# Kernel tuning notes

Hardware: AMD Instinct MI355X
Metric: run time of the kernel (lower is better)

Reference implementation:

```python
import jax, jax.numpy as jnp
import numpy as np

IN_F, OUT_F, GROUP, BITS = 4096, 11008, 128, 4
PACK = 32 // BITS            # 8 nibbles per int32 word
N_GROUPS = IN_F // GROUP     # 32
MASK = (1 << BITS) - 1       # 0xF
TOKENS = 2048


def setup_inputs() -> dict:
    key = jax.random.key(0)
    ks = jax.random.split(key, 6)
    x = jax.random.normal(ks[0], (TOKENS, IN_F), dtype=jnp.float32)
    qweight = jax.random.randint(ks[1], (IN_F // PACK, OUT_F), 0, 2147483647, dtype=jnp.int32)
    qzeros = jax.random.randint(ks[2], (N_GROUPS, OUT_F // PACK), 0, 2147483647, dtype=jnp.int32)
    qscales = jax.random.randint(ks[3], (N_GROUPS, OUT_F), 0, 256, dtype=jnp.int32)  # uint8 values
    qscales_zeros = jax.random.uniform(ks[4], (1, OUT_F), dtype=jnp.float32)
    qscales_scales = jax.random.uniform(ks[5], (1, OUT_F), dtype=jnp.float32) * 0.01
    g_idx = jnp.arange(IN_F, dtype=jnp.int32) // GROUP
    return dict(x=x, qweight=qweight, qzeros=qzeros, qscales=qscales,
                qscales_zeros=qscales_zeros, qscales_scales=qscales_scales, g_idx=g_idx)


def _dequantize(qweight, qzeros, qscales, qscales_zeros, qscales_scales, g_idx, dtype):
    shifts = jnp.arange(0, 32, BITS, dtype=jnp.int32)  # [8]
    # unpack weights: [in/8, 8, out] -> [in, out]
    w = (qweight[:, None, :] >> shifts[None, :, None]) & MASK
    w = w.reshape(-1, qweight.shape[-1])
    # unpack zero-points (+1 per original code): [n_groups, out/8, 8] -> [n_groups, out]
    z = (((qzeros[:, :, None] >> shifts[None, None, :]) & MASK) + 1)
    z = z.reshape(-1, qweight.shape[-1])
    # dequantize the uint8-quantized scales, then apply group-wise
    scales = (qscales.astype(dtype) - qscales_zeros) * qscales_scales  # [n_groups, out]
    return (w - z[g_idx]).astype(dtype) * scales[g_idx]                # [in, out]


def reference(x, qweight, qzeros, qscales, qscales_zeros, qscales_scales, g_idx):
    weight = _dequantize(qweight, qzeros, qscales, qscales_zeros, qscales_scales,
                         g_idx, x.dtype)
    return x @ weight  # bias disabled (disable_bias=True)
```

## Files before the change

### kernel.cpp

```cpp
#include <hip/hip_runtime.h>
#include <hip/hip_fp16.h>
#include <stdint.h>

#define IN_F   4096
#define OUT_F  11008
#define TOKENS 2048
#define BM 128
#define BN 64
#define BK 64
#define NT (IN_F / BK)
#define NGROUP 32
#define OPW (OUT_F / 8)

typedef _Float16 f16;
typedef __attribute__((ext_vector_type(2))) _Float16 f16x2;
typedef __attribute__((ext_vector_type(8))) _Float16 f16x8;
typedef __attribute__((ext_vector_type(4))) float f32x4;
typedef __attribute__((ext_vector_type(4))) int   i32x4;

typedef __attribute__((address_space(3))) uint32_t lds_u32_t;
typedef const __attribute__((address_space(1))) uint32_t glb_u32_t;

#define SB0() __builtin_amdgcn_sched_barrier(0)

static __device__ __forceinline__ void gload_lds16(const void* g, void* l) {
    __builtin_amdgcn_global_load_lds((glb_u32_t*)g, (lds_u32_t*)l, 16, 0, 0);
}

__global__ __launch_bounds__(256) void quant_x_kernel(const float* __restrict__ x,
                                                      char* __restrict__ xi,
                                                      float* __restrict__ aws) {
    __shared__ float red[4];
    const int row = blockIdx.x;
    const int tid = threadIdx.x;
    const float* xr = x + (size_t)row * IN_F + tid * 16;
    float v[16];
    #pragma unroll
    for (int p = 0; p < 4; ++p) {
        const float4 t = *reinterpret_cast<const float4*>(xr + p * 4);
        v[p * 4 + 0] = t.x; v[p * 4 + 1] = t.y; v[p * 4 + 2] = t.z; v[p * 4 + 3] = t.w;
    }
    float m = 0.f;
    #pragma unroll
    for (int p = 0; p < 16; ++p) m = fmaxf(m, fabsf(v[p]));
    #pragma unroll
    for (int off = 32; off > 0; off >>= 1) m = fmaxf(m, __shfl_xor(m, off));
    if ((tid & 63) == 0) red[tid >> 6] = m;
    __syncthreads();
    m = fmaxf(fmaxf(red[0], red[1]), fmaxf(red[2], red[3]));
    const float a   = m * (1.0f / 127.0f);
    const float inv = (m > 0.f) ? 127.0f / m : 0.f;
    if (tid == 0) aws[row] = a;
    const float MAGIC = 12582912.0f;
    uint32_t b[16];
    #pragma unroll
    for (int p = 0; p < 16; ++p)
        b[p] = __builtin_bit_cast(uint32_t, fmaf(v[p], inv, MAGIC)) & 0xFFu;
    i32x4 d;
    d[0] = (int)(b[0] | (b[2] << 8) | (b[4]  << 16) | (b[6]  << 24));
    d[1] = (int)(b[1] | (b[3] << 8) | (b[5]  << 16) | (b[7]  << 24));
    d[2] = (int)(b[8] | (b[10] << 8) | (b[12] << 16) | (b[14] << 24));
    d[3] = (int)(b[9] | (b[11] << 8) | (b[13] << 16) | (b[15] << 24));
    *reinterpret_cast<i32x4*>(xi + (size_t)row * IN_F + tid * 16) = d;
}

__global__ __launch_bounds__(256, 4) void qgemm_i8_kernel(
    const char*     __restrict__ xi,
    const float*    __restrict__ aws,
    const uint32_t* __restrict__ qweight,
    const uint32_t* __restrict__ qzeros,
    const int*      __restrict__ qscales,
    const float*    __restrict__ qscales_zeros,
    const float*    __restrict__ qscales_scales,
    float*          __restrict__ out)
{
    __shared__ __align__(16) char Ash[2][BM * BK];
    __shared__ __align__(16) char Bsh[2][BN * BK];

    const int tid  = threadIdx.x;
    const int lane = tid & 63;
    const int wid  = tid >> 6;
    const int wm   = wid >> 1;
    const int wn   = wid & 1;

    const int mt = blockIdx.x & 15;
    const int nt = blockIdx.x >> 4;
    const int m0 = mt * BM;
    const int n0 = nt * BN;

    const int colb = tid & 63;
    const int h    = tid >> 6;
    const int ncol = n0 + colb;
    const int boff = colb * BK + (h ^ ((colb >> 1) & 3)) * 16;
    const uint32_t* bptr = qweight + (size_t)(2 * h) * OUT_F + ncol;

    const int arow = tid >> 2;
    const int aunit = (tid & 3) ^ ((arow >> 1) & 3);
    const char* asrc0 = xi + (size_t)(m0 + arow) * IN_F + aunit * 16;
    const int adst0 = tid * 16, adst1 = (tid + 256) * 16;

    const int lr = lane & 15;
    const int lo = lane >> 4;
    int aoffr[4], boffr[2];
    #pragma unroll
    for (int f = 0; f < 4; ++f) {
        const int ra = wm * 64 + f * 16 + lr;
        aoffr[f] = ra * BK + ((lo ^ ((ra >> 1) & 3))) * 16;
    }
    #pragma unroll
    for (int j = 0; j < 2; ++j) {
        const int rb = wn * 32 + j * 16 + lr;
        boffr[j] = rb * BK + ((lo ^ ((rb >> 1) & 3))) * 16;
    }
    const int cread0 = n0 + wn * 32 + lr;
    const int cread1 = cread0 + 16;
    float qszr[2], qssr[2];
    qszr[0] = qscales_zeros[cread0]; qssr[0] = qscales_scales[cread0];
    qszr[1] = qscales_zeros[cread1]; qssr[1] = qscales_scales[cread1];

    f32x4 acc[4][2];
    #pragma unroll
    for (int i = 0; i < 4; ++i)
        #pragma unroll
        for (int j = 0; j < 2; ++j) {
            f32x4 z = {0.f, 0.f, 0.f, 0.f};
            acc[i][j] = z;
        }
    i32x4 D[4][2];

    auto load_bw = [&](int t_, uint32_t* w) {
        const uint32_t* p = bptr + (size_t)t_ * 8 * OUT_F;
        w[0] = p[0];
        w[1] = p[OUT_F];
    };
    auto mk_kz = [&](uint32_t zw_) -> uint32_t {
        const uint32_t znib = (zw_ >> ((ncol & 7) * 4)) & 0xFu;
        return (127u - znib) * 0x01010101u;
    };
    auto stage_B = [&](int buf, const uint32_t* w, uint32_t kz) {
        i32x4 d;
        d[0] = (int)((((w[0]      ) & 0x0F0F0F0Fu) + kz) ^ 0x80808080u);
        d[1] = (int)((((w[0] >> 4 ) & 0x0F0F0F0Fu) + kz) ^ 0x80808080u);
        d[2] = (int)((((w[1]      ) & 0x0F0F0F0Fu) + kz) ^ 0x80808080u);
        d[3] = (int)((((w[1] >> 4 ) & 0x0F0F0F0Fu) + kz) ^ 0x80808080u);
        *reinterpret_cast<i32x4*>(&Bsh[buf][boff]) = d;
    };
    auto stage_A = [&](int buf, int t_) {
        gload_lds16(asrc0 + (size_t)t_ * BK, &Ash[buf][adst0]);
        gload_lds16(asrc0 + (size_t)t_ * BK + (size_t)64 * IN_F, &Ash[buf][adst1]);
    };

    uint32_t wE[2], wO[2];
    uint32_t zwE, zwO;
    int sfE[2], sfO[2];

    {
        uint32_t w00[2];
        load_bw(0, w00);
        const uint32_t zw0 = qzeros[ncol >> 3];
        stage_A(0, 0);
        stage_B(0, w00, mk_kz(zw0));
        load_bw(1, wE);
        zwE = qzeros[ncol >> 3];
        sfE[0] = qscales[cread0];
        sfE[1] = qscales[cread1];
        asm volatile("s_waitcnt vmcnt(0)" ::: "memory");
        asm volatile("s_waitcnt lgkmcnt(0)" ::: "memory");
        __builtin_amdgcn_s_barrier();
    }

#define BODY(C, T, WC, ZC, SFC, WL, ZL, SFL, ODD)                                 \
  {                                                                               \
    const int tn1_ = ((T) + 1 < NT) ? (T) + 1 : NT - 1;                           \
    const int tn2_ = ((T) + 2 < NT) ? (T) + 2 : NT - 1;                           \
    const int gz_  = ((T) + 2) >> 1 < NGROUP ? ((T) + 2) >> 1 : NGROUP - 1;       \
    const int gs_  = ((T) + 1) >> 1 < NGROUP ? ((T) + 1) >> 1 : NGROUP - 1;       \
    stage_B((C) ^ 1, WC, mk_kz(ZC));                                              \
    stage_A((C) ^ 1, tn1_);                                                       \
    SB0();                                                                        \
    load_bw(tn2_, WL);                                                            \
    ZL = qzeros[(size_t)gz_ * OPW + (ncol >> 3)];                                 \
    SFL[0] = qscales[(size_t)gs_ * OUT_F + cread0];                               \
    SFL[1] = qscales[(size_t)gs_ * OUT_F + cread1];                               \
    SB0();                                                                        \
    {                                                                             \
      i32x4 af[4], bf[2];                                                         \
      _Pragma("unroll") for (int f = 0; f < 4; ++f)                               \
        af[f] = *reinterpret_cast<const i32x4*>(&Ash[C][aoffr[f]]);               \
      _Pragma("unroll") for (int j = 0; j < 2; ++j)                               \
        bf[j] = *reinterpret_cast<const i32x4*>(&Bsh[C][boffr[j]]);               \
      __builtin_amdgcn_s_setprio(1);                                              \
      if (ODD) {                                                                  \
        _Pragma("unroll") for (int i = 0; i < 4; ++i)                             \
          _Pragma("unroll") for (int j = 0; j < 2; ++j)                           \
            D[i][j] = __builtin_amdgcn_mfma_i32_16x16x64_i8(af[i], bf[j],         \
                                                            D[i][j], 0, 0, 0);   \
      } else {                                                                    \
        _Pragma("unroll") for (int i = 0; i < 4; ++i)                             \
          _Pragma("unroll") for (int j = 0; j < 2; ++j) {                         \
            i32x4 z0_ = {0, 0, 0, 0};                                             \
            D[i][j] = __builtin_amdgcn_mfma_i32_16x16x64_i8(af[i], bf[j],         \
                                                            z0_, 0, 0, 0);       \
          }                                                                       \
      }                                                                           \
      __builtin_amdgcn_s_setprio(0);                                              \
    }                                                                             \
    if (ODD) {                                                                    \
      float scur_[2];                                                             \
      _Pragma("unroll") for (int j = 0; j < 2; ++j)                               \
        scur_[j] = ((float)SFC[j] - qszr[j]) * qssr[j];                           \
      _Pragma("unroll") for (int i = 0; i < 4; ++i)                               \
        _Pragma("unroll") for (int j = 0; j < 2; ++j) {                           \
          acc[i][j].x += scur_[j] * (float)D[i][j][0];                            \
          acc[i][j].y += scur_[j] * (float)D[i][j][1];                            \
          acc[i][j].z += scur_[j] * (float)D[i][j][2];                            \
          acc[i][j].w += scur_[j] * (float)D[i][j][3];                            \
        }                                                                         \
    }                                                                             \
    asm volatile("s_waitcnt vmcnt(5)" ::: "memory");                              \
    asm volatile("s_waitcnt lgkmcnt(0)" ::: "memory");                            \
    __builtin_amdgcn_s_barrier();                                                 \
  }

    for (int t = 0; t < NT; t += 2) {
        BODY(0, t,     wE, zwE, sfE, wO, zwO, sfO, false)
        BODY(1, t + 1, wO, zwO, sfO, wE, zwE, sfE, true)
    }
#undef BODY

    const int orow = m0 + wm * 64 + lo * 4;
    const int ocol = n0 + wn * 32 + lr;
    #pragma unroll
    for (int i = 0; i < 4; ++i)
        #pragma unroll
        for (int j = 0; j < 2; ++j)
            #pragma unroll
            for (int r = 0; r < 4; ++r) {
                const int rr = orow + i * 16 + r;
                out[(size_t)rr * OUT_F + ocol + j * 16] = aws[rr] * acc[i][j][r];
            }
}

static __device__ __forceinline__ f16x8 dequant8(uint32_t w, f16x2 sv, f16x2 zv) {
    uint32_t p0 = (w & 0x000F000Fu) | 0x64006400u;
    uint32_t p1 = ((w >> 4)  & 0x000F000Fu) | 0x64006400u;
    uint32_t p2 = ((w >> 8)  & 0x000F000Fu) | 0x64006400u;
    uint32_t p3 = ((w >> 12) & 0x000F000Fu) | 0x64006400u;
    f16x2 h0 = (__builtin_bit_cast(f16x2, p0) + zv) * sv;
    f16x2 h1 = (__builtin_bit_cast(f16x2, p1) + zv) * sv;
    f16x2 h2 = (__builtin_bit_cast(f16x2, p2) + zv) * sv;
    f16x2 h3 = (__builtin_bit_cast(f16x2, p3) + zv) * sv;
    f16x8 o;
    o[0] = h0[0]; o[1] = h0[1]; o[2] = h1[0]; o[3] = h1[1];
    o[4] = h2[0]; o[5] = h2[1]; o[6] = h3[0]; o[7] = h3[1];
    return o;
}

__global__ __launch_bounds__(512, 4) void qgemm_f16_fb(
    const float* __restrict__ x, const uint32_t* __restrict__ qweight,
    const uint32_t* __restrict__ qzeros, const int* __restrict__ qscales,
    const float* __restrict__ qscales_zeros, const float* __restrict__ qscales_scales,
    float* __restrict__ out)
{
    __shared__ __align__(16) f16 heap[2][256 * 64];
    f16* const Ab0 = &heap[0][0];
    f16* const Ab1 = &heap[1][0];
    f16* const Bb0 = &heap[0][128 * 64];
    f16* const Bb1 = &heap[1][128 * 64];
    const int tid = threadIdx.x, lane = tid & 63, wid = tid >> 6;
    const int kg = wid >> 2, wm = (wid >> 1) & 1, wn = wid & 1;
    const int mt = blockIdx.x & 15, nt = blockIdx.x >> 4;
    const int m0 = mt * 128, n0 = nt * 128;
    const int colb = tid & 127, og2 = (tid >> 7) << 1, ncol = n0 + colb;
    const float ssv = qscales_scales[ncol], qzssv = qscales_zeros[ncol] * ssv;
    int bo[2];
    #pragma unroll
    for (int r = 0; r < 2; ++r) bo[r] = colb * 64 + ((og2 + r) ^ (colb & 7)) * 8;
    const uint32_t* bptr = qweight + (size_t)og2 * OUT_F + ncol;
    const int arow = tid >> 3, aoct = (tid & 7) ^ (arow & 7);
    const float* fsrc0 = x + (size_t)(m0 + arow) * IN_F + aoct * 8;
    const int aoff0 = tid * 8, aoff1 = (tid + 512) * 8;
    const int lr = lane & 15, lo = lane >> 4, koct = kg * 4 + lo;
    int offA[4], offB[4];
    #pragma unroll
    for (int f = 0; f < 4; ++f) {
        const int ra = wm * 64 + f * 16 + lr;
        offA[f] = ra * 64 + (koct ^ (ra & 7)) * 8;
        const int rb = wn * 64 + f * 16 + lr;
        offB[f] = rb * 64 + (koct ^ (rb & 7)) * 8;
    }
    f32x4 acc[4][4];
    #pragma unroll
    for (int i = 0; i < 4; ++i)
        #pragma unroll
        for (int j = 0; j < 4; ++j) { f32x4 z = {0,0,0,0}; acc[i][j] = z; }
    auto load_bw = [&](int t_, uint32_t* w) {
        const uint32_t* p = bptr + (size_t)t_ * 8 * OUT_F;
        w[0] = p[0]; w[1] = p[OUT_F];
    };
    auto mkc = [&](f16x2& sv_, f16x2& zv_, int sw_, uint32_t zw_) {
        const float sf = (float)sw_ * ssv - qzssv;
        const int z = (int)((zw_ >> ((ncol & 7) * 4)) & 0xFu);
        const f16 sh = (f16)sf, zh = (f16)(float)(-(1025 + z));
        sv_[0] = sh; sv_[1] = sh; zv_[0] = zh; zv_[1] = zh;
    };
    auto stage_B = [&](f16* Bb, const uint32_t* w, f16x2 sv_, f16x2 zv_) {
        *reinterpret_cast<f16x8*>(&Bb[bo[0]]) = dequant8(w[0], sv_, zv_);
        *reinterpret_cast<f16x8*>(&Bb[bo[1]]) = dequant8(w[1], sv_, zv_);
    };
    auto stage_A = [&](f16* Ab, int t_) {
        #pragma unroll
        for (int i = 0; i < 2; ++i) {
            const float* p = fsrc0 + (size_t)t_ * 64 + (size_t)(64 * i) * IN_F;
            const float4 v0 = *reinterpret_cast<const float4*>(p);
            const float4 v1 = *reinterpret_cast<const float4*>(p + 4);
            f16x8 v;
            v[0] = (f16)v0.x; v[1] = (f16)v1.x; v[2] = (f16)v0.y; v[3] = (f16)v1.y;
            v[4] = (f16)v0.z; v[5] = (f16)v1.z; v[6] = (f16)v0.w; v[7] = (f16)v1.w;
            *reinterpret_cast<f16x8*>(&Ab[i == 0 ? aoff0 : aoff1]) = v;
        }
    };
    auto compute = [&](const f16* Ab, const f16* Bb) {
        f16x8 af[4], bf[4];
        #pragma unroll
        for (int f = 0; f < 4; ++f) af[f] = *reinterpret_cast<const f16x8*>(&Ab[offA[f]]);
        #pragma unroll
        for (int f = 0; f < 4; ++f) bf[f] = *reinterpret_cast<const f16x8*>(&Bb[offB[f]]);
        #pragma unroll
        for (int i = 0; i < 4; ++i)
            #pragma unroll
            for (int j = 0; j < 4; ++j)
                acc[i][j] = __builtin_amdgcn_mfma_f32_16x16x32_f16(af[i], bf[j], acc[i][j], 0, 0, 0);
    };
    uint32_t wcur[2], wnxt[2];
    int swN; uint32_t zwN;
    f16x2 sv, zv, svN, zvN;
    {
        uint32_t w0[2];
        load_bw(0, w0);
        const int sw0 = qscales[ncol];
        const uint32_t zw0 = qzeros[ncol >> 3];
        stage_A(Ab0, 0);
        load_bw(1, wcur);
        swN = qscales[OUT_F + ncol]; zwN = qzeros[OPW + (ncol >> 3)];
        mkc(sv, zv, sw0, zw0);
        stage_B(Bb0, w0, sv, zv);
        asm volatile("s_waitcnt lgkmcnt(0)" ::: "memory");
        __builtin_amdgcn_s_barrier();
    }
    for (int t = 0; t < 64; t += 2) {
        mkc(svN, zvN, swN, zwN);
        stage_B(Bb1, wcur, sv, zv);
        stage_A(Ab1, t + 1);
        load_bw(t + 2 < 64 ? t + 2 : 63, wnxt);
        {
            const int g2 = (t >> 1) + 2 < NGROUP ? (t >> 1) + 2 : NGROUP - 1;
            swN = qscales[(size_t)g2 * OUT_F + ncol];
            zwN = qzeros[(size_t)g2 * OPW + (ncol >> 3)];
        }
        compute(Ab0, Bb0);
        asm volatile("s_waitcnt lgkmcnt(0)" ::: "memory");
        __builtin_amdgcn_s_barrier();
        sv = svN; zv = zvN;
        stage_B(Bb0, wnxt, sv, zv);
        stage_A(Ab0, t + 2 < 64 ? t + 2 : 63);
        load_bw(t + 3 < 64 ? t + 3 : 63, wcur);
        compute(Ab1, Bb1);
        asm volatile("s_waitcnt lgkmcnt(0)" ::: "memory");
        __builtin_amdgcn_s_barrier();
    }
    __syncthreads();
    f32x4* scratch = reinterpret_cast<f32x4*>(&heap[0][0]);
    const int wpos = wid & 3;
    #pragma unroll
    for (int hh = 0; hh < 2; ++hh) {
        if (kg == 1) {
            #pragma unroll
            for (int di = 0; di < 2; ++di)
                #pragma unroll
                for (int j = 0; j < 4; ++j)
                    scratch[wpos * 512 + (di * 4 + j) * 64 + lane] = acc[2 * hh + di][j];
        }
        __syncthreads();
        if (kg == 0) {
            #pragma unroll
            for (int di = 0; di < 2; ++di)
                #pragma unroll
                for (int j = 0; j < 4; ++j) {
                    const f32x4 p = scratch[wpos * 512 + (di * 4 + j) * 64 + lane];
                    acc[2 * hh + di][j].x += p.x; acc[2 * hh + di][j].y += p.y;
                    acc[2 * hh + di][j].z += p.z; acc[2 * hh + di][j].w += p.w;
                }
        }
        __syncthreads();
    }
    if (kg == 0) {
        const int orow = m0 + wm * 64 + lo * 4;
        const int ocol = n0 + wn * 64 + lr;
        #pragma unroll
        for (int i = 0; i < 4; ++i)
            #pragma unroll
            for (int j = 0; j < 4; ++j)
                #pragma unroll
                for (int r = 0; r < 4; ++r)
                    out[(size_t)(orow + i * 16 + r) * OUT_F + ocol + j * 16] = acc[i][j][r];
    }
}

extern "C" void kernel_launch(void* const* d_in, const int* in_sizes, int n_in,
                              void* d_out, int out_size, void* d_ws, size_t ws_size,
                              hipStream_t stream) {
    const float*    xp  = (const float*)d_in[0];
    const uint32_t* qw  = (const uint32_t*)d_in[1];
    const uint32_t* qz  = (const uint32_t*)d_in[2];
    const int*      qs  = (const int*)d_in[3];
    const float*    qsz = (const float*)d_in[4];
    const float*    qss = (const float*)d_in[5];
    float* outp = (float*)d_out;

    const size_t need = (size_t)TOKENS * IN_F + (size_t)TOKENS * 4;

    if (ws_size >= need) {
        char*  xi  = (char*)d_ws;
        float* aws = (float*)(xi + (size_t)TOKENS * IN_F);
        quant_x_kernel<<<TOKENS, 256, 0, stream>>>(xp, xi, aws);
        const int grid = (TOKENS / BM) * (OUT_F / BN);
        qgemm_i8_kernel<<<grid, 256, 0, stream>>>(xi, aws, qw, qz, qs, qsz, qss, outp);
    } else {
        const int gridf = (TOKENS / 128) * (OUT_F / 128);
        qgemm_f16_fb<<<gridf, 512, 0, stream>>>(xp, qw, qz, qs, qsz, qss, outp);
    }
}
```

Before: 179.7 us.

## Widen N tile to 128 and switch int8 GEMM to 32x32x32 MFMA

```diff
diff --git a/kernel.cpp b/kernel.cpp
--- a/kernel.cpp
+++ b/kernel.cpp
@@ -6,7 +6,7 @@
 #define OUT_F  11008
 #define TOKENS 2048
 #define BM 128
-#define BN 64
+#define BN 128
 #define BK 64
 #define NT (IN_F / BK)
 #define NGROUP 32
@@ -17,6 +17,8 @@
 typedef __attribute__((ext_vector_type(8))) _Float16 f16x8;
 typedef __attribute__((ext_vector_type(4))) float f32x4;
 typedef __attribute__((ext_vector_type(4))) int   i32x4;
+typedef __attribute__((ext_vector_type(16))) int  i32x16;
+typedef __attribute__((ext_vector_type(16))) float f32x16;
 
 typedef __attribute__((address_space(3))) uint32_t lds_u32_t;
 typedef const __attribute__((address_space(1))) uint32_t glb_u32_t;
@@ -64,7 +66,7 @@
     *reinterpret_cast<i32x4*>(xi + (size_t)row * IN_F + tid * 16) = d;
 }
 
-__global__ __launch_bounds__(256, 4) void qgemm_i8_kernel(
+__global__ __launch_bounds__(256, 3) void qgemm_i8_kernel(
     const char*     __restrict__ xi,
     const float*    __restrict__ aws,
     const uint32_t* __restrict__ qweight,
@@ -80,90 +82,99 @@
     const int tid  = threadIdx.x;
     const int lane = tid & 63;
     const int wid  = tid >> 6;
-    const int wm   = wid >> 1;
-    const int wn   = wid & 1;
+    const int wvm  = wid >> 1;
+    const int wvn  = wid & 1;
+    const int l31  = lane & 31;
+    const int hl   = lane >> 5;
 
     const int mt = blockIdx.x & 15;
     const int nt = blockIdx.x >> 4;
     const int m0 = mt * BM;
     const int n0 = nt * BN;
 
-    const int colb = tid & 63;
-    const int h    = tid >> 6;
+    const int colb = tid & 127;
+    const int p    = tid >> 7;
     const int ncol = n0 + colb;
-    const int boff = colb * BK + (h ^ ((colb >> 1) & 3)) * 16;
-    const uint32_t* bptr = qweight + (size_t)(2 * h) * OUT_F + ncol;
-
-    const int arow = tid >> 2;
+    const int bst0 = colb * BK + ((p)     ^ ((colb >> 1) & 3)) * 16;
+    const int bst1 = colb * BK + ((p + 2) ^ ((colb >> 1) & 3)) * 16;
+    const uint32_t* bptr = qweight + (size_t)(2 * p) * OUT_F + ncol;
+
+    const int arow  = tid >> 2;
     const int aunit = (tid & 3) ^ ((arow >> 1) & 3);
     const char* asrc0 = xi + (size_t)(m0 + arow) * IN_F + aunit * 16;
     const int adst0 = tid * 16, adst1 = (tid + 256) * 16;
 
-    const int lr = lane & 15;
-    const int lo = lane >> 4;
-    int aoffr[4], boffr[2];
-    #pragma unroll
-    for (int f = 0; f < 4; ++f) {
-        const int ra = wm * 64 + f * 16 + lr;
-        aoffr[f] = ra * BK + ((lo ^ ((ra >> 1) & 3))) * 16;
-    }
+    int aoffr[2][2], boffr[2][2], cread[2];
+    #pragma unroll
+    for (int rb = 0; rb < 2; ++rb)
+        #pragma unroll
+        for (int ks = 0; ks < 2; ++ks) {
+            const int ra = wvm * 64 + rb * 32 + l31;
+            aoffr[rb][ks] = ra * BK + ((ks * 2 + hl) ^ ((ra >> 1) & 3)) * 16;
+            const int cbcol = wvn * 64 + rb * 32 + l31;
+            boffr[rb][ks] = cbcol * BK + ((ks * 2 + hl) ^ ((cbcol >> 1) & 3)) * 16;
+        }
+    cread[0] = n0 + wvn * 64 + l31;
+    cread[1] = cread[0] + 32;
+    float qszr[2], qssr[2];
     #pragma unroll
     for (int j = 0; j < 2; ++j) {
-        const int rb = wn * 32 + j * 16 + lr;
-        boffr[j] = rb * BK + ((lo ^ ((rb >> 1) & 3))) * 16;
-    }
-    const int cread0 = n0 + wn * 32 + lr;
-    const int cread1 = cread0 + 16;
-    float qszr[2], qssr[2];
-    qszr[0] = qscales_zeros[cread0]; qssr[0] = qscales_scales[cread0];
-    qszr[1] = qscales_zeros[cread1]; qssr[1] = qscales_scales[cread1];
-
-    f32x4 acc[4][2];
-    #pragma unroll
-    for (int i = 0; i < 4; ++i)
-        #pragma unroll
-        for (int j = 0; j < 2; ++j) {
-            f32x4 z = {0.f, 0.f, 0.f, 0.f};
-            acc[i][j] = z;
-        }
-    i32x4 D[4][2];
+        qszr[j] = qscales_zeros[cread[j]];
+        qssr[j] = qscales_scales[cread[j]];
+    }
+
+    f32x16 acc[2][2];
+    #pragma unroll
+    for (int i = 0; i < 2; ++i)
+        #pragma unroll
+        for (int j = 0; j < 2; ++j)
+            #pragma unroll
+            for (int r = 0; r < 16; ++r) acc[i][j][r] = 0.f;
+    i32x16 D[2][2];
 
     auto load_bw = [&](int t_, uint32_t* w) {
-        const uint32_t* p = bptr + (size_t)t_ * 8 * OUT_F;
-        w[0] = p[0];
-        w[1] = p[OUT_F];
+        const uint32_t* p_ = bptr + (size_t)t_ * 8 * OUT_F;
+        w[0] = p_[0];
+        w[1] = p_[OUT_F];
+        w[2] = p_[(size_t)4 * OUT_F];
+        w[3] = p_[(size_t)5 * OUT_F];
     };
     auto mk_kz = [&](uint32_t zw_) -> uint32_t {
         const uint32_t znib = (zw_ >> ((ncol & 7) * 4)) & 0xFu;
         return (127u - znib) * 0x01010101u;
     };
     auto stage_B = [&](int buf, const uint32_t* w, uint32_t kz) {
-        i32x4 d;
-        d[0] = (int)((((w[0]      ) & 0x0F0F0F0Fu) + kz) ^ 0x80808080u);
-        d[1] = (int)((((w[0] >> 4 ) & 0x0F0F0F0Fu) + kz) ^ 0x80808080u);
-        d[2] = (int)((((w[1]      ) & 0x0F0F0F0Fu) + kz) ^ 0x80808080u);
-        d[3] = (int)((((w[1] >> 4 ) & 0x0F0F0F0Fu) + kz) ^ 0x80808080u);
-        *reinterpret_cast<i32x4*>(&Bsh[buf][boff]) = d;
+        i32x4 d0, d1;
+        d0[0] = (int)((((w[0]     ) & 0x0F0F0F0Fu) + kz) ^ 0x80808080u);
+        d0[1] = (int)((((w[0] >> 4) & 0x0F0F0F0Fu) + kz) ^ 0x80808080u);
+        d0[2] = (int)((((w[1]     ) & 0x0F0F0F0Fu) + kz) ^ 0x80808080u);
+        d0[3] = (int)((((w[1] >> 4) & 0x0F0F0F0Fu) + kz) ^ 0x80808080u);
+        d1[0] = (int)((((w[2]     ) & 0x0F0F0F0Fu) + kz) ^ 0x80808080u);
+        d1[1] = (int)((((w[2] >> 4) & 0x0F0F0F0Fu) + kz) ^ 0x80808080u);
+        d1[2] = (int)((((w[3]     ) & 0x0F0F0F0Fu) + kz) ^ 0x80808080u);
+        d1[3] = (int)((((w[3] >> 4) & 0x0F0F0F0Fu) + kz) ^ 0x80808080u);
+        *reinterpret_cast<i32x4*>(&Bsh[buf][bst0]) = d0;
+        *reinterpret_cast<i32x4*>(&Bsh[buf][bst1]) = d1;
     };
     auto stage_A = [&](int buf, int t_) {
         gload_lds16(asrc0 + (size_t)t_ * BK, &Ash[buf][adst0]);
         gload_lds16(asrc0 + (size_t)t_ * BK + (size_t)64 * IN_F, &Ash[buf][adst1]);
     };
 
-    uint32_t wE[2], wO[2];
+    uint32_t wE[4], wO[4];
     uint32_t zwE, zwO;
     int sfE[2], sfO[2];
 
     {
-        uint32_t w00[2];
+        uint32_t w00[4];
         load_bw(0, w00);
         const uint32_t zw0 = qzeros[ncol >> 3];
         stage_A(0, 0);
         stage_B(0, w00, mk_kz(zw0));
         load_bw(1, wE);
         zwE = qzeros[ncol >> 3];
-        sfE[0] = qscales[cread0];
-        sfE[1] = qscales[cread1];
+        sfE[0] = qscales[cread[0]];
+        sfE[1] = qscales[cread[1]];
         asm volatile("s_waitcnt vmcnt(0)" ::: "memory");
         asm volatile("s_waitcnt lgkmcnt(0)" ::: "memory");
         __builtin_amdgcn_s_barrier();
@@ -180,44 +191,39 @@
     SB0();                                                                        \
     load_bw(tn2_, WL);                                                            \
     ZL = qzeros[(size_t)gz_ * OPW + (ncol >> 3)];                                 \
-    SFL[0] = qscales[(size_t)gs_ * OUT_F + cread0];                               \
-    SFL[1] = qscales[(size_t)gs_ * OUT_F + cread1];                               \
+    SFL[0] = qscales[(size_t)gs_ * OUT_F + cread[0]];                             \
+    SFL[1] = qscales[(size_t)gs_ * OUT_F + cread[1]];                             \
     SB0();                                                                        \
-    {                                                                             \
-      i32x4 af[4], bf[2];                                                         \
-      _Pragma("unroll") for (int f = 0; f < 4; ++f)                               \
-        af[f] = *reinterpret_cast<const i32x4*>(&Ash[C][aoffr[f]]);               \
-      _Pragma("unroll") for (int j = 0; j < 2; ++j)                               \
-        bf[j] = *reinterpret_cast<const i32x4*>(&Bsh[C][boffr[j]]);               \
+    _Pragma("unroll") for (int ks = 0; ks < 2; ++ks) {                            \
+      i32x4 af[2], bf[2];                                                         \
+      _Pragma("unroll") for (int rb = 0; rb < 2; ++rb)                            \
+        af[rb] = *reinterpret_cast<const i32x4*>(&Ash[C][aoffr[rb][ks]]);         \
+      _Pragma("unroll") for (int cb = 0; cb < 2; ++cb)                            \
+        bf[cb] = *reinterpret_cast<const i32x4*>(&Bsh[C][boffr[cb][ks]]);         \
       __builtin_amdgcn_s_setprio(1);                                              \
-      if (ODD) {                                                                  \
-        _Pragma("unroll") for (int i = 0; i < 4; ++i)                             \
-          _Pragma("unroll") for (int j = 0; j < 2; ++j)                           \
-            D[i][j] = __builtin_amdgcn_mfma_i32_16x16x64_i8(af[i], bf[j],         \
-                                                            D[i][j], 0, 0, 0);   \
-      } else {                                                                    \
-        _Pragma("unroll") for (int i = 0; i < 4; ++i)                             \
-          _Pragma("unroll") for (int j = 0; j < 2; ++j) {                         \
-            i32x4 z0_ = {0, 0, 0, 0};                                             \
-            D[i][j] = __builtin_amdgcn_mfma_i32_16x16x64_i8(af[i], bf[j],         \
-                                                            z0_, 0, 0, 0);       \
+      _Pragma("unroll") for (int rb = 0; rb < 2; ++rb)                            \
+        _Pragma("unroll") for (int cb = 0; cb < 2; ++cb) {                        \
+          if (!(ODD) && ks == 0) {                                                \
+            i32x16 z0_ = {};                                                      \
+            D[rb][cb] = __builtin_amdgcn_mfma_i32_32x32x32_i8(af[rb], bf[cb],     \
+                                                              z0_, 0, 0, 0);     \
+          } else {                                                                \
+            D[rb][cb] = __builtin_amdgcn_mfma_i32_32x32x32_i8(af[rb], bf[cb],     \
+                                                         D[rb][cb], 0, 0, 0);    \
           }                                                                       \
-      }                                                                           \
+        }                                                                         \
       __builtin_amdgcn_s_setprio(0);                                              \
     }                                                                             \
     if (ODD) {                                                                    \
       float scur_[2];                                                             \
       _Pragma("unroll") for (int j = 0; j < 2; ++j)                               \
         scur_[j] = ((float)SFC[j] - qszr[j]) * qssr[j];                           \
-      _Pragma("unroll") for (int i = 0; i < 4; ++i)                               \
-        _Pragma("unroll") for (int j = 0; j < 2; ++j) {                           \
-          acc[i][j].x += scur_[j] * (float)D[i][j][0];                            \
-          acc[i][j].y += scur_[j] * (float)D[i][j][1];                            \
-          acc[i][j].z += scur_[j] * (float)D[i][j][2];                            \
-          acc[i][j].w += scur_[j] * (float)D[i][j][3];                            \
-        }                                                                         \
+      _Pragma("unroll") for (int rb = 0; rb < 2; ++rb)                            \
+        _Pragma("unroll") for (int cb = 0; cb < 2; ++cb)                          \
+          _Pragma("unroll") for (int r = 0; r < 16; ++r)                          \
+            acc[rb][cb][r] += scur_[cb] * (float)D[rb][cb][r];                    \
     }                                                                             \
-    asm volatile("s_waitcnt vmcnt(5)" ::: "memory");                              \
+    asm volatile("s_waitcnt vmcnt(7)" ::: "memory");                              \
     asm volatile("s_waitcnt lgkmcnt(0)" ::: "memory");                            \
     __builtin_amdgcn_s_barrier();                                                 \
   }
@@ -228,16 +234,15 @@
     }
 #undef BODY
 
-    const int orow = m0 + wm * 64 + lo * 4;
-    const int ocol = n0 + wn * 32 + lr;
-    #pragma unroll
-    for (int i = 0; i < 4; ++i)
-        #pragma unroll
-        for (int j = 0; j < 2; ++j)
-            #pragma unroll
-            for (int r = 0; r < 4; ++r) {
-                const int rr = orow + i * 16 + r;
-                out[(size_t)rr * OUT_F + ocol + j * 16] = aws[rr] * acc[i][j][r];
+    #pragma unroll
+    for (int rb = 0; rb < 2; ++rb)
+        #pragma unroll
+        for (int cb = 0; cb < 2; ++cb)
+            #pragma unroll
+            for (int r = 0; r < 16; ++r) {
+                const int rr = m0 + wvm * 64 + rb * 32 + (r & 3) + 8 * (r >> 2) + 4 * hl;
+                const int cc = n0 + wvn * 64 + cb * 32 + l31;
+                out[(size_t)rr * OUT_F + cc] = aws[rr] * acc[rb][cb][r];
             }
 }
 
```

Measured after the change: 238.4 us. 32.7% more time.

## Double K tile to one full quantization group per pipeline stage

Applied to the files above, without the earlier changes.

```diff
diff --git a/kernel.cpp b/kernel.cpp
--- a/kernel.cpp
+++ b/kernel.cpp
@@ -7,7 +7,7 @@
 #define TOKENS 2048
 #define BM 128
 #define BN 64
-#define BK 64
+#define BK 128
 #define NT (IN_F / BK)
 #define NGROUP 32
 #define OPW (OUT_F / 8)
@@ -91,26 +91,35 @@
     const int colb = tid & 63;
     const int h    = tid >> 6;
     const int ncol = n0 + colb;
-    const int boff = colb * BK + (h ^ ((colb >> 1) & 3)) * 16;
+    const int bst0 = colb * BK + ((h)     ^ (colb & 7)) * 16;
+    const int bst1 = colb * BK + ((h + 4) ^ (colb & 7)) * 16;
     const uint32_t* bptr = qweight + (size_t)(2 * h) * OUT_F + ncol;
 
-    const int arow = tid >> 2;
-    const int aunit = (tid & 3) ^ ((arow >> 1) & 3);
-    const char* asrc0 = xi + (size_t)(m0 + arow) * IN_F + aunit * 16;
-    const int adst0 = tid * 16, adst1 = (tid + 256) * 16;
+    const char* asrcb = xi + (size_t)m0 * IN_F;
+    int asoff[4], adst[4];
+    #pragma unroll
+    for (int i = 0; i < 4; ++i) {
+        const int cid = i * 256 + tid;
+        const int row = cid >> 3, slot = cid & 7;
+        asoff[i] = (int)((size_t)row * IN_F) + (slot ^ (row & 7)) * 16;
+        adst[i]  = cid * 16;
+    }
 
     const int lr = lane & 15;
     const int lo = lane >> 4;
-    int aoffr[4], boffr[2];
-    #pragma unroll
-    for (int f = 0; f < 4; ++f) {
-        const int ra = wm * 64 + f * 16 + lr;
-        aoffr[f] = ra * BK + ((lo ^ ((ra >> 1) & 3))) * 16;
-    }
-    #pragma unroll
-    for (int j = 0; j < 2; ++j) {
-        const int rb = wn * 32 + j * 16 + lr;
-        boffr[j] = rb * BK + ((lo ^ ((rb >> 1) & 3))) * 16;
+    int aoffr[2][4], boffr[2][2];
+    #pragma unroll
+    for (int ks = 0; ks < 2; ++ks) {
+        #pragma unroll
+        for (int f = 0; f < 4; ++f) {
+            const int ra = wm * 64 + f * 16 + lr;
+            aoffr[ks][f] = ra * BK + ((ks * 4 + lo) ^ (ra & 7)) * 16;
+        }
+        #pragma unroll
+        for (int j = 0; j < 2; ++j) {
+            const int rb = wn * 32 + j * 16 + lr;
+            boffr[ks][j] = rb * BK + ((ks * 4 + lo) ^ (rb & 7)) * 16;
+        }
     }
     const int cread0 = n0 + wn * 32 + lr;
     const int cread1 = cread0 + 16;
@@ -129,39 +138,47 @@
     i32x4 D[4][2];
 
     auto load_bw = [&](int t_, uint32_t* w) {
-        const uint32_t* p = bptr + (size_t)t_ * 8 * OUT_F;
+        const uint32_t* p = bptr + (size_t)t_ * 16 * OUT_F;
         w[0] = p[0];
         w[1] = p[OUT_F];
+        w[2] = p[(size_t)8 * OUT_F];
+        w[3] = p[(size_t)9 * OUT_F];
     };
     auto mk_kz = [&](uint32_t zw_) -> uint32_t {
         const uint32_t znib = (zw_ >> ((ncol & 7) * 4)) & 0xFu;
         return (127u - znib) * 0x01010101u;
     };
     auto stage_B = [&](int buf, const uint32_t* w, uint32_t kz) {
-        i32x4 d;
-        d[0] = (int)((((w[0]      ) & 0x0F0F0F0Fu) + kz) ^ 0x80808080u);
-        d[1] = (int)((((w[0] >> 4 ) & 0x0F0F0F0Fu) + kz) ^ 0x80808080u);
-        d[2] = (int)((((w[1]      ) & 0x0F0F0F0Fu) + kz) ^ 0x80808080u);
-        d[3] = (int)((((w[1] >> 4 ) & 0x0F0F0F0Fu) + kz) ^ 0x80808080u);
-        *reinterpret_cast<i32x4*>(&Bsh[buf][boff]) = d;
+        i32x4 d0, d1;
+        d0[0] = (int)((((w[0]     ) & 0x0F0F0F0Fu) + kz) ^ 0x80808080u);
+        d0[1] = (int)((((w[0] >> 4) & 0x0F0F0F0Fu) + kz) ^ 0x80808080u);
+        d0[2] = (int)((((w[1]     ) & 0x0F0F0F0Fu) + kz) ^ 0x80808080u);
+        d0[3] = (int)((((w[1] >> 4) & 0x0F0F0F0Fu) + kz) ^ 0x80808080u);
+        d1[0] = (int)((((w[2]     ) & 0x0F0F0F0Fu) + kz) ^ 0x80808080u);
+        d1[1] = (int)((((w[2] >> 4) & 0x0F0F0F0Fu) + kz) ^ 0x80808080u);
+        d1[2] = (int)((((w[3]     ) & 0x0F0F0F0Fu) + kz) ^ 0x80808080u);
+        d1[3] = (int)((((w[3] >> 4) & 0x0F0F0F0Fu) + kz) ^ 0x80808080u);
+        *reinterpret_cast<i32x4*>(&Bsh[buf][bst0]) = d0;
+        *reinterpret_cast<i32x4*>(&Bsh[buf][bst1]) = d1;
     };
     auto stage_A = [&](int buf, int t_) {
-        gload_lds16(asrc0 + (size_t)t_ * BK, &Ash[buf][adst0]);
-        gload_lds16(asrc0 + (size_t)t_ * BK + (size_t)64 * IN_F, &Ash[buf][adst1]);
-    };
-
-    uint32_t wE[2], wO[2];
+        #pragma unroll
+        for (int i = 0; i < 4; ++i)
+            gload_lds16(asrcb + (size_t)t_ * BK + asoff[i], &Ash[buf][adst[i]]);
+    };
+
+    uint32_t wE[4], wO[4];
     uint32_t zwE, zwO;
     int sfE[2], sfO[2];
 
     {
-        uint32_t w00[2];
+        uint32_t w00[4];
         load_bw(0, w00);
         const uint32_t zw0 = qzeros[ncol >> 3];
         stage_A(0, 0);
         stage_B(0, w00, mk_kz(zw0));
         load_bw(1, wE);
-        zwE = qzeros[ncol >> 3];
+        zwE = qzeros[OPW + (ncol >> 3)];
         sfE[0] = qscales[cread0];
         sfE[1] = qscales[cread1];
         asm volatile("s_waitcnt vmcnt(0)" ::: "memory");
@@ -169,43 +186,39 @@
         __builtin_amdgcn_s_barrier();
     }
 
-#define BODY(C, T, WC, ZC, SFC, WL, ZL, SFL, ODD)                                 \
+#define BODY(C, T, WC, ZC, SFC, WL, ZL, SFL)                                      \
   {                                                                               \
     const int tn1_ = ((T) + 1 < NT) ? (T) + 1 : NT - 1;                           \
     const int tn2_ = ((T) + 2 < NT) ? (T) + 2 : NT - 1;                           \
-    const int gz_  = ((T) + 2) >> 1 < NGROUP ? ((T) + 2) >> 1 : NGROUP - 1;       \
-    const int gs_  = ((T) + 1) >> 1 < NGROUP ? ((T) + 1) >> 1 : NGROUP - 1;       \
     stage_B((C) ^ 1, WC, mk_kz(ZC));                                              \
     stage_A((C) ^ 1, tn1_);                                                       \
     SB0();                                                                        \
     load_bw(tn2_, WL);                                                            \
-    ZL = qzeros[(size_t)gz_ * OPW + (ncol >> 3)];                                 \
-    SFL[0] = qscales[(size_t)gs_ * OUT_F + cread0];                               \
-    SFL[1] = qscales[(size_t)gs_ * OUT_F + cread1];                               \
+    ZL = qzeros[(size_t)tn2_ * OPW + (ncol >> 3)];                                \
+    SFL[0] = qscales[(size_t)tn1_ * OUT_F + cread0];                              \
+    SFL[1] = qscales[(size_t)tn1_ * OUT_F + cread1];                              \
     SB0();                                                                        \
-    {                                                                             \
+    _Pragma("unroll") for (int ks = 0; ks < 2; ++ks) {                            \
       i32x4 af[4], bf[2];                                                         \
       _Pragma("unroll") for (int f = 0; f < 4; ++f)                               \
-        af[f] = *reinterpret_cast<const i32x4*>(&Ash[C][aoffr[f]]);               \
+        af[f] = *reinterpret_cast<const i32x4*>(&Ash[C][aoffr[ks][f]]);           \
       _Pragma("unroll") for (int j = 0; j < 2; ++j)                               \
-        bf[j] = *reinterpret_cast<const i32x4*>(&Bsh[C][boffr[j]]);               \
+        bf[j] = *reinterpret_cast<const i32x4*>(&Bsh[C][boffr[ks][j]]);           \
       __builtin_amdgcn_s_setprio(1);                                              \
-      if (ODD) {                                                                  \
-        _Pragma("unroll") for (int i = 0; i < 4; ++i)                             \
-          _Pragma("unroll") for (int j = 0; j < 2; ++j)                           \
-            D[i][j] = __builtin_amdgcn_mfma_i32_16x16x64_i8(af[i], bf[j],         \
-                                                            D[i][j], 0, 0, 0);   \
-      } else {                                                                    \
-        _Pragma("unroll") for (int i = 0; i < 4; ++i)                             \
-          _Pragma("unroll") for (int j = 0; j < 2; ++j) {                         \
+      _Pragma("unroll") for (int i = 0; i < 4; ++i)                               \
+        _Pragma("unroll") for (int j = 0; j < 2; ++j) {                           \
+          if (ks == 0) {                                                          \
             i32x4 z0_ = {0, 0, 0, 0};                                             \
             D[i][j] = __builtin_amdgcn_mfma_i32_16x16x64_i8(af[i], bf[j],         \
                                                             z0_, 0, 0, 0);       \
+          } else {                                                                \
+            D[i][j] = __builtin_amdgcn_mfma_i32_16x16x64_i8(af[i], bf[j],         \
+                                                            D[i][j], 0, 0, 0);   \
           }                                                                       \
-      }                                                                           \
+        }                                                                         \
       __builtin_amdgcn_s_setprio(0);                                              \
     }                                                                             \
-    if (ODD) {                                                                    \
+    {                                                                             \
       float scur_[2];                                                             \
       _Pragma("unroll") for (int j = 0; j < 2; ++j)                               \
         scur_[j] = ((float)SFC[j] - qszr[j]) * qssr[j];                           \
@@ -217,14 +230,14 @@
           acc[i][j].w += scur_[j] * (float)D[i][j][3];                            \
         }                                                                         \
     }                                                                             \
-    asm volatile("s_waitcnt vmcnt(5)" ::: "memory");                              \
+    asm volatile("s_waitcnt vmcnt(7)" ::: "memory");                              \
     asm volatile("s_waitcnt lgkmcnt(0)" ::: "memory");                            \
     __builtin_amdgcn_s_barrier();                                                 \
   }
 
     for (int t = 0; t < NT; t += 2) {
-        BODY(0, t,     wE, zwE, sfE, wO, zwO, sfO, false)
-        BODY(1, t + 1, wO, zwO, sfO, wE, zwE, sfE, true)
+        BODY(0, t,     wE, zwE, sfE, wO, zwO, sfO)
+        BODY(1, t + 1, wO, zwO, sfO, wE, zwE, sfE)
     }
 #undef BODY
 
```

New measurement: 215.6 us. 1.2x slower.
